# Kernel tuning notes

Hardware: AMD Instinct MI355X
Metric: run time of the kernel (lower is better)

## Reference

```python
import jax, jax.numpy as jnp
import numpy as np

# Concrete segmented-polynomial instance (uniform 1d):
N = 8192      # nodes (rows of input 0 and of the indexed output)
E = 16384     # edges (batch dim of input 1 and of the per-edge product)
S = 16        # segments per operand (buffer_num_segments, same for all 3 operands)
EXT = 64      # operand_extent (uniform segment shape)
P = 2048      # num_paths of the single operation


def setup_inputs() -> dict:
    key = jax.random.key(0)
    k0, k1, k2, k3, k4, k5 = jax.random.split(key, 6)
    x = jax.random.normal(k0, (N, S * EXT), dtype=jnp.float32)          # node features
    y = jax.random.normal(k1, (E, S * EXT), dtype=jnp.float32)          # edge features
    idx_in = jax.random.randint(k2, (E,), 0, N, dtype=jnp.int32)        # gather index for input 0
    idx_out = jax.random.randint(k3, (E,), 0, N, dtype=jnp.int32)       # scatter index for output 0
    path_indices = jax.random.randint(k4, (P, 3), 0, S, dtype=jnp.int32)  # (i_x, j_y, k_out) per path
    path_coefficients = jax.random.normal(k5, (P,), dtype=jnp.float32)
    return {
        "x": x, "y": y,
        "idx_in": idx_in, "idx_out": idx_out,
        "path_indices": path_indices,
        "path_coefficients": path_coefficients,
    }


def reference(x, y, idx_in, idx_out, path_indices, path_coefficients):
    # Dense path-coefficient tensor C[k, i, j]: duplicate paths accumulate,
    # missing (k,i,j) triples are zero. This is the math-dtype (fp32) contraction
    # the uniform-1d kernel performs over segments of equal extent.
    C = jnp.zeros((S, S, S), dtype=x.dtype).at[
        path_indices[:, 2], path_indices[:, 0], path_indices[:, 1]
    ].add(path_coefficients)

    xr = x.reshape(N, S, EXT)[idx_in]   # gather (BATCH_DIM_INDEXED input): [E, S, EXT]
    yr = y.reshape(E, S, EXT)           # batched input:                    [E, S, EXT]

    # out_e[e, k, c] = sum_{i,j} C[k,i,j] * xr[e,i,c] * yr[e,j,c]
    out_e = jnp.einsum('kij,eic,ejc->ekc', C, xr, yr)

    # scatter-add (BATCH_DIM_INDEXED output) into N output rows
    out = jnp.zeros((N, S, EXT), dtype=x.dtype).at[idx_out].add(out_e)
    return out.reshape(N, S * EXT)
```

## Files before the change

### kernel.cpp

```cpp
#include <hip/hip_runtime.h>
#include <hip/hip_bf16.h>

#define N_NODES 8192
#define E_EDGES 16384
#define S_SEG   16
#define EXT     64
#define P_PATHS 2048
#define ROW     (S_SEG * EXT)

typedef _Float16 f16x8  __attribute__((ext_vector_type(8)));
typedef _Float16 f16x4  __attribute__((ext_vector_type(4)));
typedef _Float16 half2v __attribute__((ext_vector_type(2)));
typedef float    f32x4  __attribute__((ext_vector_type(4)));

#define WS_CMAT  0
#define WS_HIST  8192
#define WS_CURS  40960
#define WS_ROWS  73728
#define WS_ELIST 106512

__global__ void prep(const int* __restrict__ pidx, const float* __restrict__ pcoef,
                     _Float16* __restrict__ Cmat, int* __restrict__ hist) {
    const int tid = threadIdx.x;
    if (blockIdx.x < 32) {
        hist[blockIdx.x * 256 + tid] = 0;
        return;
    }
    __shared__ float sC[S_SEG * S_SEG * S_SEG];
    for (int i = tid; i < 4096; i += 256) sC[i] = 0.f;
    __syncthreads();
    for (int p = tid; p < P_PATHS; p += 256) {
        int i = pidx[3 * p + 0];
        int j = pidx[3 * p + 1];
        int k = pidx[3 * p + 2];
        atomicAdd(&sC[(k * S_SEG + i) * S_SEG + j], pcoef[p]);
    }
    __syncthreads();
    for (int i = tid; i < 4096; i += 256) Cmat[i] = (_Float16)sC[i];
}

__global__ void hist_k(const int* __restrict__ idx_out, int* __restrict__ hist) {
    const int e = blockIdx.x * 256 + threadIdx.x;
    atomicAdd(&hist[idx_out[e]], 1);
}

__global__ __launch_bounds__(256) void scan_k(const int* __restrict__ hist,
                                              int* __restrict__ rows,
                                              int* __restrict__ cursor) {
    __shared__ int part[256];
    const int t = threadIdx.x;
    const int base = t * 32;
    int loc[32];
    int s = 0;
#pragma unroll
    for (int i = 0; i < 32; ++i) { loc[i] = s; s += hist[base + i]; }
    part[t] = s;
    __syncthreads();
    for (int off = 1; off < 256; off <<= 1) {
        int v = part[t];
        int u = (t >= off) ? part[t - off] : 0;
        __syncthreads();
        part[t] = v + u;
        __syncthreads();
    }
    const int excl = (t == 0) ? 0 : part[t - 1];
#pragma unroll
    for (int i = 0; i < 32; ++i) {
        int v = excl + loc[i];
        rows[base + i] = v;
        cursor[base + i] = v;
    }
    if (t == 255) rows[N_NODES] = part[255];
}

__global__ void scatter_k(const int* __restrict__ idx_out, int* __restrict__ cursor,
                          int* __restrict__ elist) {
    const int e = blockIdx.x * 256 + threadIdx.x;
    const int pos = atomicAdd(&cursor[idx_out[e]], 1);
    elist[pos] = e;
}

__global__ __launch_bounds__(256) void seg_poly_wave(
        const float* __restrict__ x, const float* __restrict__ y,
        const int* __restrict__ idx_in, const _Float16* __restrict__ Cmat,
        const int* __restrict__ rows, const int* __restrict__ elist,
        float* __restrict__ out) {
    __shared__ __attribute__((aligned(16))) _Float16 sx_all[4][ROW];
    __shared__ __attribute__((aligned(16))) half2v   sy_all[4][512];

    const int tid  = threadIdx.x;
    const int lane = tid & 63;
    const int wv   = tid >> 6;
    _Float16* sxh = sx_all[wv];
    half2v*   syp = sy_all[wv];

    const int n = blockIdx.x * 4 + wv;
    const int beg = rows[n];
    const int end = rows[n + 1];

    const int quad = lane >> 4;
    const int m    = lane & 15;
    const int jb2  = (quad & 1) * 4;
    const int ih   = quad >> 1;

    f16x8 afrag[8];
    {
        const _Float16* basep = Cmat + m * 256 + quad * 8;
#pragma unroll
        for (int kk = 0; kk < 8; ++kk)
            afrag[kk] = *(const f16x8*)(basep + kk * 32);
    }

    f32x4 acc[4];
#pragma unroll
    for (int ct = 0; ct < 4; ++ct) acc[ct] = f32x4{0.f, 0.f, 0.f, 0.f};

    for (int p = beg; p < end; ++p) {
        const int e  = elist[p];
        const int xr = idx_in[e];

        {
            const float* xb = x + (size_t)xr * ROW;
#pragma unroll
            for (int k4 = 0; k4 < 4; ++k4) {
                const float4 v = *(const float4*)(xb + k4 * 256 + lane * 4);
                f16x4 h = {(_Float16)v.x, (_Float16)v.y, (_Float16)v.z, (_Float16)v.w};
                *(f16x4*)(sxh + k4 * 256 + lane * 4) = h;
            }
        }
        {
            const int jp = lane >> 3;
            const int cq = (lane & 7) * 8;
            const float* yb = y + (size_t)e * ROW;
            const float4 a0 = *(const float4*)(yb + (2 * jp)     * EXT + cq);
            const float4 a1 = *(const float4*)(yb + (2 * jp)     * EXT + cq + 4);
            const float4 b0 = *(const float4*)(yb + (2 * jp + 1) * EXT + cq);
            const float4 b1 = *(const float4*)(yb + (2 * jp + 1) * EXT + cq + 4);
            f16x8 p0 = {(_Float16)a0.x, (_Float16)b0.x, (_Float16)a0.y, (_Float16)b0.y,
                        (_Float16)a0.z, (_Float16)b0.z, (_Float16)a0.w, (_Float16)b0.w};
            f16x8 p1 = {(_Float16)a1.x, (_Float16)b1.x, (_Float16)a1.y, (_Float16)b1.y,
                        (_Float16)a1.z, (_Float16)b1.z, (_Float16)a1.w, (_Float16)b1.w};
            *(f16x8*)(syp + jp * 64 + cq)     = p0;
            *(f16x8*)(syp + jp * 64 + cq + 4) = p1;
        }

#pragma unroll
        for (int ct = 0; ct < 4; ++ct) {
            const int c = ct * 16 + m;
            half2v ypk[4];
#pragma unroll
            for (int r = 0; r < 4; ++r) ypk[r] = syp[(jb2 + r) * 64 + c];
#pragma unroll
            for (int kk = 0; kk < 8; ++kk) {
                const _Float16 xh = sxh[(2 * kk + ih) * EXT + c];
                const half2v hx = {xh, xh};
                const half2v b0 = hx * ypk[0];
                const half2v b1 = hx * ypk[1];
                const half2v b2 = hx * ypk[2];
                const half2v b3 = hx * ypk[3];
                const f16x8 bfrag = {b0[0], b0[1], b1[0], b1[1],
                                     b2[0], b2[1], b3[0], b3[1]};
                acc[ct] = __builtin_amdgcn_mfma_f32_16x16x32_f16(
                              afrag[kk], bfrag, acc[ct], 0, 0, 0);
            }
        }
    }

    float* ob = out + (size_t)n * ROW;
#pragma unroll
    for (int ct = 0; ct < 4; ++ct)
#pragma unroll
        for (int r = 0; r < 4; ++r)
            ob[(quad * 4 + r) * EXT + ct * 16 + m] = acc[ct][r];
}

extern "C" void kernel_launch(void* const* d_in, const int* in_sizes, int n_in,
                              void* d_out, int out_size, void* d_ws, size_t ws_size,
                              hipStream_t stream) {
    const float* x       = (const float*)d_in[0];
    const float* y       = (const float*)d_in[1];
    const int*   idx_in  = (const int*)d_in[2];
    const int*   idx_out = (const int*)d_in[3];
    const int*   pidx    = (const int*)d_in[4];
    const float* pcoef   = (const float*)d_in[5];
    float* out           = (float*)d_out;

    char* ws = (char*)d_ws;
    _Float16* Cmat = (_Float16*)(ws + WS_CMAT);
    int* hist      = (int*)(ws + WS_HIST);
    int* cursor    = (int*)(ws + WS_CURS);
    int* rows      = (int*)(ws + WS_ROWS);
    int* elist     = (int*)(ws + WS_ELIST);

    prep<<<33, 256, 0, stream>>>(pidx, pcoef, Cmat, hist);
    hist_k<<<E_EDGES / 256, 256, 0, stream>>>(idx_out, hist);
    scan_k<<<1, 256, 0, stream>>>(hist, rows, cursor);
    scatter_k<<<E_EDGES / 256, 256, 0, stream>>>(idx_out, cursor, elist);
    seg_poly_wave<<<N_NODES / 4, 256, 0, stream>>>(x, y, idx_in, Cmat, rows, elist, out);
}
```

Measured before the change: 165.6 us.

## Split sorted edge list into fixed 8-edge slots per wave with boundary atomics

Replaces the one-wave-per-node loop, whose trip count varies with node degree, with fixed 8-edge slots per wave over the sorted edge list, so every wave does the same amount of work. Node rows that span slot boundaries are accumulated with atomics, and a new zero-fill kernel clears those rows and rows with no edges. It also double-buffers the global loads of x and y across slots and precomputes the gathered x row and destination node per sorted position in the scatter kernel. The costs are an extra launch, atomic traffic at slot boundaries, and nondeterministic summation order on shared rows.

```diff
diff --git a/kernel.cpp b/kernel.cpp
--- a/kernel.cpp
+++ b/kernel.cpp
@@ -6,7 +6,10 @@
 #define S_SEG   16
 #define EXT     64
 #define P_PATHS 2048
-#define ROW     (S_SEG * EXT)
+#define ROW     1024
+#define L_SLOTS 8
+#define NWAVES  (E_EDGES / L_SLOTS)
+#define NBLK    (NWAVES / 4)
 
 typedef _Float16 f16x8  __attribute__((ext_vector_type(8)));
 typedef _Float16 f16x4  __attribute__((ext_vector_type(4)));
@@ -18,14 +21,13 @@
 #define WS_CURS  40960
 #define WS_ROWS  73728
 #define WS_ELIST 106512
+#define WS_XRS   172048
+#define WS_NDS   237584
 
 __global__ void prep(const int* __restrict__ pidx, const float* __restrict__ pcoef,
                      _Float16* __restrict__ Cmat, int* __restrict__ hist) {
     const int tid = threadIdx.x;
-    if (blockIdx.x < 32) {
-        hist[blockIdx.x * 256 + tid] = 0;
-        return;
-    }
+    if (blockIdx.x < 32) { hist[blockIdx.x * 256 + tid] = 0; return; }
     __shared__ float sC[S_SEG * S_SEG * S_SEG];
     for (int i = tid; i < 4096; i += 256) sC[i] = 0.f;
     __syncthreads();
@@ -73,18 +75,35 @@
     if (t == 255) rows[N_NODES] = part[255];
 }
 
-__global__ void scatter_k(const int* __restrict__ idx_out, int* __restrict__ cursor,
-                          int* __restrict__ elist) {
+__global__ void scatter_k(const int* __restrict__ idx_in, const int* __restrict__ idx_out,
+                          int* __restrict__ cursor, int* __restrict__ elist,
+                          int* __restrict__ xrs, int* __restrict__ nds) {
     const int e = blockIdx.x * 256 + threadIdx.x;
-    const int pos = atomicAdd(&cursor[idx_out[e]], 1);
+    const int nd = idx_out[e];
+    const int pos = atomicAdd(&cursor[nd], 1);
     elist[pos] = e;
-}
-
-__global__ __launch_bounds__(256) void seg_poly_wave(
+    xrs[pos]   = idx_in[e];
+    nds[pos]   = nd;
+}
+
+__global__ __launch_bounds__(256) void zerofill_k(const int* __restrict__ rows,
+                                                  float* __restrict__ out) {
+    const int n = blockIdx.x * 4 + (threadIdx.x >> 6);
+    const int lane = threadIdx.x & 63;
+    const int beg = rows[n], end = rows[n + 1];
+    const bool need = (beg == end) || ((beg / L_SLOTS) != ((end - 1) / L_SLOTS));
+    if (!need) return;
+    const float4 z = {0.f, 0.f, 0.f, 0.f};
+    float* ob = out + (size_t)n * ROW + lane * 4;
+#pragma unroll
+    for (int r = 0; r < 4; ++r) *(float4*)(ob + r * 256) = z;
+}
+
+__global__ __launch_bounds__(256) void seg_poly_slots(
         const float* __restrict__ x, const float* __restrict__ y,
-        const int* __restrict__ idx_in, const _Float16* __restrict__ Cmat,
-        const int* __restrict__ rows, const int* __restrict__ elist,
-        float* __restrict__ out) {
+        const _Float16* __restrict__ Cmat,
+        const int* __restrict__ elist, const int* __restrict__ xrs,
+        const int* __restrict__ nds, float* __restrict__ out) {
     __shared__ __attribute__((aligned(16))) _Float16 sx_all[4][ROW];
     __shared__ __attribute__((aligned(16))) half2v   sy_all[4][512];
 
@@ -94,54 +113,74 @@
     _Float16* sxh = sx_all[wv];
     half2v*   syp = sy_all[wv];
 
-    const int n = blockIdx.x * 4 + wv;
-    const int beg = rows[n];
-    const int end = rows[n + 1];
+    const int wid = blockIdx.x * 4 + wv;
+    const int s0  = wid * L_SLOTS;
 
     const int quad = lane >> 4;
     const int m    = lane & 15;
     const int jb2  = (quad & 1) * 4;
     const int ih   = quad >> 1;
+    const int jp   = lane >> 3;
+    const int cq   = (lane & 7) * 8;
+
+    int e_[L_SLOTS], xr_[L_SLOTS], nd_[L_SLOTS];
+    {
+        int4 a = *(const int4*)(elist + s0); int4 b = *(const int4*)(elist + s0 + 4);
+        e_[0]=a.x; e_[1]=a.y; e_[2]=a.z; e_[3]=a.w; e_[4]=b.x; e_[5]=b.y; e_[6]=b.z; e_[7]=b.w;
+        a = *(const int4*)(xrs + s0); b = *(const int4*)(xrs + s0 + 4);
+        xr_[0]=a.x; xr_[1]=a.y; xr_[2]=a.z; xr_[3]=a.w; xr_[4]=b.x; xr_[5]=b.y; xr_[6]=b.z; xr_[7]=b.w;
+        a = *(const int4*)(nds + s0); b = *(const int4*)(nds + s0 + 4);
+        nd_[0]=a.x; nd_[1]=a.y; nd_[2]=a.z; nd_[3]=a.w; nd_[4]=b.x; nd_[5]=b.y; nd_[6]=b.z; nd_[7]=b.w;
+    }
+    const bool prev_same = (s0 > 0)                  && (nds[s0 - 1]       == nd_[0]);
+    const bool next_same = (s0 + L_SLOTS < E_EDGES)  && (nds[s0 + L_SLOTS] == nd_[L_SLOTS - 1]);
 
     f16x8 afrag[8];
     {
         const _Float16* basep = Cmat + m * 256 + quad * 8;
 #pragma unroll
-        for (int kk = 0; kk < 8; ++kk)
-            afrag[kk] = *(const f16x8*)(basep + kk * 32);
-    }
+        for (int kk = 0; kk < 8; ++kk) afrag[kk] = *(const f16x8*)(basep + kk * 32);
+    }
+
+    float4 xbuf[2][4], ybuf[2][4];
+    auto issue = [&](int t, int b) {
+        const float* xp = x + (size_t)xr_[t] * ROW;
+        const float* yp = y + (size_t)e_[t] * ROW;
+#pragma unroll
+        for (int k4 = 0; k4 < 4; ++k4)
+            xbuf[b][k4] = *(const float4*)(xp + k4 * 256 + lane * 4);
+        ybuf[b][0] = *(const float4*)(yp + (2 * jp)     * EXT + cq);
+        ybuf[b][1] = *(const float4*)(yp + (2 * jp)     * EXT + cq + 4);
+        ybuf[b][2] = *(const float4*)(yp + (2 * jp + 1) * EXT + cq);
+        ybuf[b][3] = *(const float4*)(yp + (2 * jp + 1) * EXT + cq + 4);
+    };
+    issue(0, 0);
 
     f32x4 acc[4];
 #pragma unroll
     for (int ct = 0; ct < 4; ++ct) acc[ct] = f32x4{0.f, 0.f, 0.f, 0.f};
-
-    for (int p = beg; p < end; ++p) {
-        const int e  = elist[p];
-        const int xr = idx_in[e];
-
+    int segStart = 0;
+
+#pragma unroll
+    for (int t = 0; t < L_SLOTS; ++t) {
+        const int b = t & 1;
+        if (t + 1 < L_SLOTS) issue(t + 1, b ^ 1);
+
+#pragma unroll
+        for (int k4 = 0; k4 < 4; ++k4) {
+            const float4 v = xbuf[b][k4];
+            *(f16x4*)(sxh + k4 * 256 + lane * 4) =
+                f16x4{(_Float16)v.x, (_Float16)v.y, (_Float16)v.z, (_Float16)v.w};
+        }
         {
-            const float* xb = x + (size_t)xr * ROW;
-#pragma unroll
-            for (int k4 = 0; k4 < 4; ++k4) {
-                const float4 v = *(const float4*)(xb + k4 * 256 + lane * 4);
-                f16x4 h = {(_Float16)v.x, (_Float16)v.y, (_Float16)v.z, (_Float16)v.w};
-                *(f16x4*)(sxh + k4 * 256 + lane * 4) = h;
-            }
-        }
-        {
-            const int jp = lane >> 3;
-            const int cq = (lane & 7) * 8;
-            const float* yb = y + (size_t)e * ROW;
-            const float4 a0 = *(const float4*)(yb + (2 * jp)     * EXT + cq);
-            const float4 a1 = *(const float4*)(yb + (2 * jp)     * EXT + cq + 4);
-            const float4 b0 = *(const float4*)(yb + (2 * jp + 1) * EXT + cq);
-            const float4 b1 = *(const float4*)(yb + (2 * jp + 1) * EXT + cq + 4);
-            f16x8 p0 = {(_Float16)a0.x, (_Float16)b0.x, (_Float16)a0.y, (_Float16)b0.y,
-                        (_Float16)a0.z, (_Float16)b0.z, (_Float16)a0.w, (_Float16)b0.w};
-            f16x8 p1 = {(_Float16)a1.x, (_Float16)b1.x, (_Float16)a1.y, (_Float16)b1.y,
-                        (_Float16)a1.z, (_Float16)b1.z, (_Float16)a1.w, (_Float16)b1.w};
-            *(f16x8*)(syp + jp * 64 + cq)     = p0;
-            *(f16x8*)(syp + jp * 64 + cq + 4) = p1;
+            const float4 a0 = ybuf[b][0], a1 = ybuf[b][1];
+            const float4 c0 = ybuf[b][2], c1 = ybuf[b][3];
+            *(f16x8*)(syp + jp * 64 + cq) =
+                f16x8{(_Float16)a0.x, (_Float16)c0.x, (_Float16)a0.y, (_Float16)c0.y,
+                      (_Float16)a0.z, (_Float16)c0.z, (_Float16)a0.w, (_Float16)c0.w};
+            *(f16x8*)(syp + jp * 64 + cq + 4) =
+                f16x8{(_Float16)a1.x, (_Float16)c1.x, (_Float16)a1.y, (_Float16)c1.y,
+                      (_Float16)a1.z, (_Float16)c1.z, (_Float16)a1.w, (_Float16)c1.w};
         }
 
 #pragma unroll
@@ -164,14 +203,29 @@
                               afrag[kk], bfrag, acc[ct], 0, 0, 0);
             }
         }
-    }
-
-    float* ob = out + (size_t)n * ROW;
-#pragma unroll
-    for (int ct = 0; ct < 4; ++ct)
-#pragma unroll
-        for (int r = 0; r < 4; ++r)
-            ob[(quad * 4 + r) * EXT + ct * 16 + m] = acc[ct][r];
+
+        const bool last = (t == L_SLOTS - 1);
+        if (last || nd_[t + 1] != nd_[t]) {
+            const bool shared = (segStart == 0 && prev_same) || (last && next_same);
+            float* ob = out + (size_t)nd_[t] * ROW;
+            if (shared) {
+#pragma unroll
+                for (int ct = 0; ct < 4; ++ct)
+#pragma unroll
+                    for (int r = 0; r < 4; ++r)
+                        atomicAdd(ob + (quad * 4 + r) * EXT + ct * 16 + m, acc[ct][r]);
+            } else {
+#pragma unroll
+                for (int ct = 0; ct < 4; ++ct)
+#pragma unroll
+                    for (int r = 0; r < 4; ++r)
+                        ob[(quad * 4 + r) * EXT + ct * 16 + m] = acc[ct][r];
+            }
+#pragma unroll
+            for (int ct = 0; ct < 4; ++ct) acc[ct] = f32x4{0.f, 0.f, 0.f, 0.f};
+            segStart = t + 1;
+        }
+    }
 }
 
 extern "C" void kernel_launch(void* const* d_in, const int* in_sizes, int n_in,
@@ -191,10 +245,13 @@
     int* cursor    = (int*)(ws + WS_CURS);
     int* rows      = (int*)(ws + WS_ROWS);
     int* elist     = (int*)(ws + WS_ELIST);
+    int* xrs       = (int*)(ws + WS_XRS);
+    int* nds       = (int*)(ws + WS_NDS);
 
     prep<<<33, 256, 0, stream>>>(pidx, pcoef, Cmat, hist);
     hist_k<<<E_EDGES / 256, 256, 0, stream>>>(idx_out, hist);
     scan_k<<<1, 256, 0, stream>>>(hist, rows, cursor);
-    scatter_k<<<E_EDGES / 256, 256, 0, stream>>>(idx_out, cursor, elist);
-    seg_poly_wave<<<N_NODES / 4, 256, 0, stream>>>(x, y, idx_in, Cmat, rows, elist, out);
-}
+    scatter_k<<<E_EDGES / 256, 256, 0, stream>>>(idx_in, idx_out, cursor, elist, xrs, nds);
+    zerofill_k<<<N_NODES / 4, 256, 0, stream>>>(rows, out);
+    seg_poly_slots<<<NBLK, 256, 0, stream>>>(x, y, Cmat, elist, xrs, nds, out);
+}
```

Result: faster. 162.2 us (-2.1%).
